# Optimization experiments

Hardware: AMD Instinct MI355X
Metric: run time of the kernel (lower is better)

## Reference

```python
import jax, jax.numpy as jnp
import numpy as np

BETA, ALPHA, NS_STEPS = 0.9, 1.0, 1
D_MODEL, D_STATE, D_CONV, EXPAND = 768, 16, 4, 2
D_INNER = EXPAND * D_MODEL
DT_RANK = -(-D_MODEL // 16)  # ceil(d_model/16) = 48
B, L = 2, 1024


def setup_inputs() -> dict:
    key = jax.random.key(0)
    ks = jax.random.split(key, 8)
    s = lambda k, shape, sc=0.02: jax.random.normal(k, shape, jnp.float32) * sc
    return {
        "hidden_states": jax.random.normal(ks[0], (B, L, D_MODEL), jnp.float32),
        "in_proj_w": s(ks[1], (2 * D_INNER, D_MODEL)),
        "conv_w": s(ks[2], (D_INNER, 1, D_CONV), 0.2),
        "conv_b": jnp.zeros((D_INNER,), jnp.float32),
        "x_proj_w": s(ks[3], (DT_RANK + 2 * D_STATE, D_INNER)),
        "dt_head_w": s(ks[4], (D_INNER, DT_RANK)),
        "dt_head_b": s(ks[5], (D_INNER,), 0.1),
        "out_proj_w": s(ks[6], (D_MODEL, D_INNER)),
        "D": jnp.ones((D_INNER,), jnp.float32),
    }


def _newton_schulz(G, steps):
    """Muon-style quintic Newton-Schulz orthogonalization of (b, d, n) with d >= n."""
    a, b, c = 3.4445, -4.7750, 2.0315
    X = G / (jnp.linalg.norm(G, axis=(-2, -1), keepdims=True) + 1e-7)
    X = X.swapaxes(-2, -1)  # (b, n, d): rows <= cols
    for _ in range(steps):
        A = X @ X.swapaxes(-2, -1)       # (b, n, n) small Gram
        Bm = b * A + c * (A @ A)
        X = a * X + Bm @ X
    return X.swapaxes(-2, -1)            # back to (b, d, n)


def reference(hidden_states, in_proj_w, conv_w, conv_b, x_proj_w, dt_head_w, dt_head_b, out_proj_w, D):
    Bz, Lz, _ = hidden_states.shape
    dtype = hidden_states.dtype
    # input projection -> x, z  (B, L, d_inner) each
    xz = jnp.einsum('bld,ed->ble', hidden_states, in_proj_w)
    x, z = jnp.split(xz, 2, axis=-1)
    # causal depthwise conv over time + SiLU
    xc = jax.lax.conv_general_dilated(
        x.swapaxes(1, 2), conv_w, (1,), [(D_CONV - 1, 0)],
        dimension_numbers=('NCH', 'OIH', 'NCH'), feature_group_count=D_INNER)
    x = jax.nn.silu(xc.swapaxes(1, 2) + conv_b)  # (B, L, d_inner)
    # projections for dt / k / q
    x_dbl = jnp.einsum('bld,ed->ble', x, x_proj_w)
    dt_low, k, q = jnp.split(x_dbl, [DT_RANK, DT_RANK + D_STATE], axis=-1)
    dt = jnp.einsum('blr,dr->bld', dt_low, dt_head_w)  # (B, L, d_inner), bias applied in scan

    def step(carry, inp):
        v, h = carry  # velocity / hidden states, each (b, d_inner, d_state)
        x_t, dt_t, k_t, q_t = inp
        dt_t = jax.nn.sigmoid(dt_t + dt_head_b)                              # (b, d)
        dt_t = dt_t / (1.0 + dt_t * jnp.sum(k_t * k_t, axis=-1, keepdims=True))
        dA = 1.0 - dt_t[:, :, None] * (k_t * k_t)[:, None, :]                # (b, d, n)
        G = (dt_t * x_t)[:, :, None] * k_t[:, None, :]                       # dt * u * k
        v = BETA * v + ALPHA * _newton_schulz(G, NS_STEPS)
        h = dA * h + v
        y_t = jnp.einsum('bdn,bn->bd', h, q_t) + D * x_t
        return (v, h), y_t

    init = (jnp.zeros((Bz, D_INNER, D_STATE), dtype),
            jnp.zeros((Bz, D_INNER, D_STATE), dtype))
    xs = (x.swapaxes(0, 1), dt.swapaxes(0, 1), k.swapaxes(0, 1), q.swapaxes(0, 1))
    _, y = jax.lax.scan(step, init, xs)        # (L, B, d_inner)
    y = y.swapaxes(0, 1) * jax.nn.silu(z)      # gate
    return jnp.einsum('bld,od->blo', y, out_proj_w)
```

## Files before the change

### kernel.cpp

```cpp
#include <hip/hip_runtime.h>

#define D_MODEL 768
#define D_STATE 16
#define D_INNER 1536
#define DT_RANK 48
#define NB 2
#define LSEQ 1024
#define NROWS (NB * LSEQ)
#define CCH 16
#define CLEN (LSEQ / CCH)
#define STP 16
#define BETA_CL 1.1790185e-03f
#define OUT_ELEMS (NROWS * D_MODEL)

typedef __attribute__((ext_vector_type(4))) float f32x4;
typedef __attribute__((ext_vector_type(8))) short s16x8;
typedef __attribute__((ext_vector_type(8))) unsigned short u16x8;
typedef __attribute__((ext_vector_type(4))) unsigned short u16x4;

__device__ __forceinline__ unsigned short f2bu(float f) {
  unsigned int x = __builtin_bit_cast(unsigned int, f);
  x += 0x7fffu + ((x >> 16) & 1u);
  return (unsigned short)(x >> 16);
}

typedef __attribute__((address_space(3))) unsigned int as3u32;
typedef __attribute__((address_space(1))) const unsigned int as1u32;
__device__ __forceinline__ void gload16(const unsigned short* g, unsigned short* l) {
  __builtin_amdgcn_global_load_lds((as1u32*)g, (as3u32*)l, 16, 0, 0);
}

#define CVT_TOTAL 663552
#define Z1_GROUPS 20480
__global__ __launch_bounds__(256) void cvt5z_kernel(const float* __restrict__ s0,
                                                    const float* __restrict__ s1,
                                                    const float* __restrict__ s2,
                                                    const float* __restrict__ s3,
                                                    const float* __restrict__ s4,
                                                    unsigned short* __restrict__ d0,
                                                    unsigned short* __restrict__ d1,
                                                    unsigned short* __restrict__ d2,
                                                    unsigned short* __restrict__ d3,
                                                    unsigned short* __restrict__ d4,
                                                    float* __restrict__ z1) {
  int g = blockIdx.x * 256 + threadIdx.x;
  if (g >= CVT_TOTAL) {
    int zg = g - CVT_TOTAL;
    f32x4 zero = {0.f, 0.f, 0.f, 0.f};
    if (zg < Z1_GROUPS) {
      *(f32x4*)(z1 + zg * 8) = zero;
      *(f32x4*)(z1 + zg * 8 + 4) = zero;
    }
    return;
  }
  const float* s;
  unsigned short* d;
  int base;
  if (g < 196608)      { s = s0; d = d0; base = 0; }
  else if (g < 491520) { s = s1; d = d1; base = 196608; }
  else if (g < 506880) { s = s2; d = d2; base = 491520; }
  else if (g < 516096) { s = s3; d = d3; base = 506880; }
  else                 { s = s4; d = d4; base = 516096; }
  int i = (g - base) * 8;
  f32x4 a = *(const f32x4*)(s + i);
  f32x4 b = *(const f32x4*)(s + i + 4);
  u16x8 o;
#pragma unroll
  for (int j = 0; j < 4; j++) { o[j] = f2bu(a[j]); o[4 + j] = f2bu(b[j]); }
  *(u16x8*)(d + i) = o;
}

template <bool PARTIAL>
__global__ __launch_bounds__(256) void gemm128(const unsigned short* __restrict__ A,
                                               const unsigned short* __restrict__ B,
                                               float* __restrict__ C, int K,
                                               int lda, int ldb, int ldc, int kseg_len) {
  __shared__ __align__(16) unsigned short As[2][128 * 32];
  __shared__ __align__(16) unsigned short Bs[2][128 * 32];
  const int m0 = blockIdx.y * 128, n0 = blockIdx.x * 128;
  const int kbeg = blockIdx.z * kseg_len;
  const int kend = kbeg + kseg_len;
  const int t = threadIdx.x;
  const int wave = t >> 6, lane = t & 63;
  const int wm = wave >> 1, wn = wave & 1;
  const int quad = lane >> 4, l16 = lane & 15;
  const int srow = lane >> 2;
  const int kcol = (lane & 3) * 8;

  float* Cp = C;
  if constexpr (PARTIAL) Cp = C + (size_t)blockIdx.z * (size_t)gridDim.y * 128 * ldc;

  auto stage = [&](int bi, int k0) {
#pragma unroll
    for (int r = 0; r < 2; r++) {
      const int seg = r * 64 + wave * 16;
      gload16(A + (size_t)(m0 + seg + srow) * lda + k0 + kcol, &As[bi][seg * 32]);
      gload16(B + (size_t)(n0 + seg + srow) * ldb + k0 + kcol, &Bs[bi][seg * 32]);
    }
  };

  f32x4 acc[4][4] = {};
  stage(0, kbeg);
  __syncthreads();
  int buf = 0;
  for (int k0 = kbeg; k0 < kend; k0 += 32) {
    if (k0 + 32 < kend) stage(buf ^ 1, k0 + 32);
    s16x8 af[4], bf[4];
#pragma unroll
    for (int i = 0; i < 4; i++) {
      af[i] = *(const s16x8*)&As[buf][(wm * 64 + i * 16 + l16) * 32 + quad * 8];
      bf[i] = *(const s16x8*)&Bs[buf][(wn * 64 + i * 16 + l16) * 32 + quad * 8];
    }
#pragma unroll
    for (int mi = 0; mi < 4; mi++)
#pragma unroll
      for (int ni = 0; ni < 4; ni++)
        acc[mi][ni] = __builtin_amdgcn_mfma_f32_16x16x32_bf16(af[mi], bf[ni], acc[mi][ni], 0, 0, 0);
    __syncthreads();
    buf ^= 1;
  }
#pragma unroll
  for (int mi = 0; mi < 4; mi++)
#pragma unroll
    for (int ni = 0; ni < 4; ni++)
#pragma unroll
      for (int r = 0; r < 4; r++) {
        int row = m0 + wm * 64 + mi * 16 + quad * 4 + r;
        int col = n0 + wn * 64 + ni * 16 + l16;
        Cp[(size_t)row * ldc + col] = acc[mi][ni][r];
      }
}

__global__ __launch_bounds__(256) void reduce4_kernel(const float* __restrict__ part,
                                                      float* __restrict__ out) {
  int i4 = (blockIdx.x * 256 + threadIdx.x) * 4;
  f32x4 a = *(const f32x4*)(part + i4);
  f32x4 b = *(const f32x4*)(part + (size_t)OUT_ELEMS + i4);
  f32x4 c = *(const f32x4*)(part + (size_t)2 * OUT_ELEMS + i4);
  f32x4 d = *(const f32x4*)(part + (size_t)3 * OUT_ELEMS + i4);
  f32x4 o;
#pragma unroll
  for (int j = 0; j < 4; j++) o[j] = (a[j] + b[j]) + (c[j] + d[j]);
  *(f32x4*)(out + i4) = o;
}

template <bool AF32, bool ATOMIC>
__global__ __launch_bounds__(256) void gemm_bt(const void* __restrict__ Av,
                                               const unsigned short* __restrict__ B,
                                               float* __restrict__ C, int M, int N, int K,
                                               int lda, int ldb, int ldc, int kseg_len) {
  __shared__ __align__(16) unsigned short As[2][64][40];
  __shared__ __align__(16) unsigned short Bs[2][64][40];
  const int m0 = blockIdx.y * 64, n0 = blockIdx.x * 64;
  const int kbeg = blockIdx.z * kseg_len;
  const int kend = (kbeg + kseg_len < K) ? (kbeg + kseg_len) : K;
  const int t = threadIdx.x;
  const int wave = t >> 6, lane = t & 63;
  const int wm = wave >> 1, wn = wave & 1;
  const int quad = lane >> 4, l16 = lane & 15;
  const int srow = t >> 2;
  const int kseg = (t & 3) * 8;
  const bool va = (m0 + srow) < M, vb = (n0 + srow) < N;
  const float* Af = (const float*)Av;
  const unsigned short* Ab = (const unsigned short*)Av;
  const unsigned short* Bp = B + (size_t)(n0 + srow) * ldb;

  f32x4 ra0, ra1;
  u16x8 rab, rbb;
  auto pref = [&](int k0) {
    const int kk = k0 + kseg;
    const int krem = kend - kk;
    if constexpr (AF32) {
      const float* Ap = Af + (size_t)(m0 + srow) * lda + kk;
      if (va && krem >= 8) {
        ra0 = *(const f32x4*)Ap;
        ra1 = *(const f32x4*)(Ap + 4);
      } else {
#pragma unroll
        for (int j = 0; j < 4; j++) {
          ra0[j] = (va && j < krem) ? Ap[j] : 0.0f;
          ra1[j] = (va && j + 4 < krem) ? Ap[j + 4] : 0.0f;
        }
      }
    } else {
      const unsigned short* Ap = Ab + (size_t)(m0 + srow) * lda + kk;
      if (va && krem >= 8) {
        rab = *(const u16x8*)Ap;
      } else {
#pragma unroll
        for (int j = 0; j < 8; j++) rab[j] = (va && j < krem) ? Ap[j] : (unsigned short)0;
      }
    }
    if (vb && krem >= 8) {
      rbb = *(const u16x8*)(Bp + kk);
    } else {
#pragma unroll
      for (int j = 0; j < 8; j++) rbb[j] = (vb && j < krem) ? Bp[kk + j] : (unsigned short)0;
    }
  };
  auto tolds = [&](int bi) {
    if constexpr (AF32) {
      u16x8 oa;
#pragma unroll
      for (int j = 0; j < 4; j++) { oa[j] = f2bu(ra0[j]); oa[4 + j] = f2bu(ra1[j]); }
      *(u16x8*)&As[bi][srow][kseg] = oa;
    } else {
      *(u16x8*)&As[bi][srow][kseg] = rab;
    }
    *(u16x8*)&Bs[bi][srow][kseg] = rbb;
  };

  f32x4 acc[2][2] = {};
  pref(kbeg);
  tolds(0);
  __syncthreads();
  int buf = 0;
  for (int k0 = kbeg; k0 < kend; k0 += 32) {
    const bool more = (k0 + 32 < kend);
    if (more) pref(k0 + 32);
    s16x8 a0 = *(const s16x8*)&As[buf][wm * 32 + l16][quad * 8];
    s16x8 a1 = *(const s16x8*)&As[buf][wm * 32 + 16 + l16][quad * 8];
    s16x8 b0 = *(const s16x8*)&Bs[buf][wn * 32 + l16][quad * 8];
    s16x8 b1 = *(const s16x8*)&Bs[buf][wn * 32 + 16 + l16][quad * 8];
    acc[0][0] = __builtin_amdgcn_mfma_f32_16x16x32_bf16(a0, b0, acc[0][0], 0, 0, 0);
    acc[0][1] = __builtin_amdgcn_mfma_f32_16x16x32_bf16(a0, b1, acc[0][1], 0, 0, 0);
    acc[1][0] = __builtin_amdgcn_mfma_f32_16x16x32_bf16(a1, b0, acc[1][0], 0, 0, 0);
    acc[1][1] = __builtin_amdgcn_mfma_f32_16x16x32_bf16(a1, b1, acc[1][1], 0, 0, 0);
    if (more) tolds(buf ^ 1);
    __syncthreads();
    buf ^= 1;
  }
#pragma unroll
  for (int mi = 0; mi < 2; mi++)
#pragma unroll
    for (int ni = 0; ni < 2; ni++)
#pragma unroll
      for (int r = 0; r < 4; r++) {
        int row = m0 + wm * 32 + mi * 16 + quad * 4 + r;
        int col = n0 + wn * 32 + ni * 16 + l16;
        if (row < M && col < N) {
          if constexpr (ATOMIC)
            atomicAdd(&C[(size_t)row * ldc + col], acc[mi][ni][r]);
          else
            C[(size_t)row * ldc + col] = acc[mi][ni][r];
        }
      }
}

__global__ __launch_bounds__(256) void conv_silu_kernel(const float* __restrict__ xzp,
                                                        const float* __restrict__ cw,
                                                        const float* __restrict__ cb,
                                                        float* __restrict__ xc,
                                                        unsigned short* __restrict__ xcb) {
  int g = blockIdx.x * 256 + threadIdx.x;
  int c4 = (g % 384) * 4;
  int row = g / 384;
  int l = row & (LSEQ - 1);
  const float* x0 = xzp;
  const float* x1 = xzp + (size_t)NROWS * 3072;
  f32x4 acc = *(const f32x4*)(cb + c4);
  f32x4 w[4];
#pragma unroll
  for (int ci = 0; ci < 4; ci++) w[ci] = *(const f32x4*)(cw + (c4 + ci) * 4);
#pragma unroll
  for (int j = 0; j < 4; j++) {
    int dl = l - 3 + j;
    if (dl >= 0) {
      size_t off = (size_t)(row - 3 + j) * 3072 + c4;
      f32x4 a0 = *(const f32x4*)(x0 + off);
      f32x4 a1 = *(const f32x4*)(x1 + off);
#pragma unroll
      for (int ci = 0; ci < 4; ci++) acc[ci] = fmaf(a0[ci] + a1[ci], w[ci][j], acc[ci]);
    }
  }
  f32x4 val;
  u16x4 ob;
#pragma unroll
  for (int ci = 0; ci < 4; ci++) {
    float sg = 1.0f / (1.0f + expf(-acc[ci]));
    val[ci] = acc[ci] * sg;
    ob[ci] = f2bu(val[ci]);
  }
  *(f32x4*)(xc + (size_t)row * D_INNER + c4) = val;
  *(u16x4*)(xcb + (size_t)row * D_INNER + c4) = ob;
}

__global__ __launch_bounds__(256) void precompute_kernel(const float* __restrict__ xdbl,
                                                         float* __restrict__ dtbuf,
                                                         const float* __restrict__ xconv,
                                                         const float* __restrict__ dtb,
                                                         float* __restrict__ gammabuf,
                                                         float* __restrict__ kqbuf) {
  int row = blockIdx.x;
  int t = threadIdx.x;
  const float* xr = xdbl + (size_t)row * 80;
  float nk = 0.0f;
#pragma unroll
  for (int n = 0; n < 16; n++) { float kv = xr[48 + n]; nk += kv * kv; }
  float nupart = 0.0f;
#pragma unroll
  for (int gi = 0; gi < 2; gi++) {
    int g = gi * 256 + t;
    if (g < 384) {
      int d = g * 4;
      f32x4 draw = *(const f32x4*)(dtbuf + (size_t)row * D_INNER + d);
      f32x4 bb = *(const f32x4*)(dtb + d);
      f32x4 xcv = *(const f32x4*)(xconv + (size_t)row * D_INNER + d);
      f32x4 df;
#pragma unroll
      for (int j = 0; j < 4; j++) {
        float sg = 1.0f / (1.0f + expf(-(draw[j] + bb[j])));
        float dv = sg / (1.0f + sg * nk);
        df[j] = dv;
        float u = dv * xcv[j];
        nupart += u * u;
      }
      *(f32x4*)(dtbuf + (size_t)row * D_INNER + d) = df;
    }
  }
  __shared__ float red[4];
  float v = nupart;
#pragma unroll
  for (int off = 32; off > 0; off >>= 1) v += __shfl_xor(v, off);
  if ((t & 63) == 0) red[t >> 6] = v;
  __syncthreads();
  float nu = red[0] + red[1] + red[2] + red[3];
  float p = nu * nk;
  float s = sqrtf(p) + 1e-7f;
  float tt = p / (s * s);
  float gamma = (3.4445f + tt * (-4.7750f + 2.0315f * tt)) / s;
  if (t == 0) gammabuf[row] = gamma;
  if (t < 8)
    *(f32x4*)(kqbuf + (size_t)row * 32 + t * 4) = *(const f32x4*)(xr + 48 + t * 4);
}

__global__ __launch_bounds__(256) void scan_phase1(const float* __restrict__ xconv,
                                                   const float* __restrict__ dtbuf,
                                                   const float* __restrict__ kqbuf,
                                                   const float* __restrict__ gammabuf,
                                                   float* __restrict__ cvp,
                                                   float* __restrict__ chp,
                                                   float* __restrict__ gp,
                                                   float* __restrict__ rp) {
  __shared__ __align__(16) float xc_s[2][STP][64];
  __shared__ __align__(16) float dt_s[2][STP][64];
  __shared__ __align__(16) float kq_s[2][STP][36];
  __shared__ float g_s[2][STP];
  const int t = threadIdx.x;
  const int nq = t & 3, dloc = t >> 2;
  const int b = blockIdx.x / (24 * CCH);
  const int rem = blockIdx.x % (24 * CCH);
  const int d0 = (rem / CCH) * 64;
  const int c = rem % CCH;
  const int tbase = c * CLEN;
  const size_t ub = ((size_t)b * LSEQ + tbase) * D_INNER + d0;
  const float* kqb = kqbuf + ((size_t)b * LSEQ + tbase) * 32;
  const float* gmb = gammabuf + (size_t)b * LSEQ + tbase;
  const int prow = t >> 4, pcol = (t & 15) * 4;
  const int krow = t >> 3, kcol = (t & 7) * 4;
  f32x4 pxc, pd, pk;
  float pg;
  auto prefetch = [&](int t0) {
    size_t off = ub + (size_t)(t0 + prow) * D_INNER + pcol;
    pxc = *(const f32x4*)(xconv + off);
    pd = *(const f32x4*)(dtbuf + off);
    if (t < 128) pk = *(const f32x4*)(kqb + (size_t)(t0 + krow) * 32 + kcol);
    if (t < STP) pg = gmb[t0 + t];
  };
  auto writelds = [&](int bi) {
    *(f32x4*)&xc_s[bi][prow][pcol] = pxc;
    *(f32x4*)&dt_s[bi][prow][pcol] = pd;
    if (t < 128) *(f32x4*)&kq_s[bi][krow][kcol] = pk;
    if (t < STP) g_s[bi][t] = pg;
  };
  f32x4 v = {0.f, 0.f, 0.f, 0.f}, h = {0.f, 0.f, 0.f, 0.f};
  f32x4 g = {0.f, 0.f, 0.f, 0.f}, r = {1.f, 1.f, 1.f, 1.f};
  float bt = 0.9f;
  prefetch(0);
  writelds(0);
  __syncthreads();
  int buf = 0;
  for (int t0 = 0; t0 < CLEN; t0 += STP) {
    const bool more = (t0 + STP < CLEN);
    if (more) prefetch(t0 + STP);
#pragma unroll 4
    for (int s = 0; s < STP; s++) {
      float dtf = dt_s[buf][s][dloc];
      float u = g_s[buf][s] * dtf * xc_s[buf][s][dloc];
#pragma unroll
      for (int j = 0; j < 4; j++) {
        float kj = kq_s[buf][s][nq * 4 + j];
        v[j] = fmaf(0.9f, v[j], u * kj);
        float a = fmaf(-dtf * kj, kj, 1.0f);
        h[j] = fmaf(a, h[j], v[j]);
        r[j] *= a;
        g[j] = fmaf(a, g[j], bt);
      }
      bt *= 0.9f;
    }
    if (more) writelds(buf ^ 1);
    __syncthreads();
    buf ^= 1;
  }
  size_t o = (((size_t)b * CCH + c) * D_INNER + d0 + dloc) * 16 + nq * 4;
  *(f32x4*)(cvp + o) = v;
  *(f32x4*)(chp + o) = h;
  *(f32x4*)(gp + o) = g;
  *(f32x4*)(rp + o) = r;
}

__global__ __launch_bounds__(256) void scan_phase2(const float* __restrict__ cvp,
                                                   const float* __restrict__ chp,
                                                   float* __restrict__ gp,
                                                   float* __restrict__ rp) {
  int i4 = (blockIdx.x * 256 + threadIdx.x) * 4;
  int b = i4 / (D_INNER * 16);
  int rem = i4 % (D_INNER * 16);
  f32x4 v0 = {0.f, 0.f, 0.f, 0.f}, h0 = {0.f, 0.f, 0.f, 0.f};
#pragma unroll
  for (int c = 0; c < CCH; c++) {
    size_t o = ((size_t)(b * CCH + c)) * (D_INNER * 16) + rem;
    f32x4 cv = *(const f32x4*)(cvp + o);
    f32x4 ch = *(const f32x4*)(chp + o);
    f32x4 gg = *(const f32x4*)(gp + o);
    f32x4 rr = *(const f32x4*)(rp + o);
    *(f32x4*)(gp + o) = v0;
    *(f32x4*)(rp + o) = h0;
#pragma unroll
    for (int j = 0; j < 4; j++) {
      float v0n = fmaf(BETA_CL, v0[j], cv[j]);
      float h0n = fmaf(gg[j], v0[j], fmaf(rr[j], h0[j], ch[j]));
      v0[j] = v0n;
      h0[j] = h0n;
    }
  }
}

__global__ __launch_bounds__(256) void scan_phase3(const float* __restrict__ dtbuf,
                                                   const float* __restrict__ kqbuf,
                                                   const float* __restrict__ gammabuf,
                                                   const float* __restrict__ gp,
                                                   const float* __restrict__ rp,
                                                   const float* __restrict__ xconv,
                                                   const float* __restrict__ xzp,
                                                   const float* __restrict__ Dp,
                                                   unsigned short* __restrict__ ygb) {
  __shared__ __align__(16) float xc_s[2][STP][64];
  __shared__ __align__(16) float dt_s[2][STP][64];
  __shared__ __align__(16) float z_s[2][STP][64];
  __shared__ __align__(16) float kq_s[2][STP][36];
  __shared__ float g_s[2][STP];
  const int t = threadIdx.x;
  const int nq = t & 3, dloc = t >> 2;
  const int b = blockIdx.x / (24 * CCH);
  const int rem = blockIdx.x % (24 * CCH);
  const int d0 = (rem / CCH) * 64;
  const int c = rem % CCH;
  const int tbase = c * CLEN;
  const size_t ub = ((size_t)b * LSEQ + tbase) * D_INNER + d0;
  const float* kqb = kqbuf + ((size_t)b * LSEQ + tbase) * 32;
  const float* gmb = gammabuf + (size_t)b * LSEQ + tbase;
  const float* z0 = xzp + ((size_t)b * LSEQ + tbase) * 3072 + 1536 + d0;
  const float* z1 = z0 + (size_t)NROWS * 3072;
  unsigned short* y_p = ygb + (size_t)b * LSEQ * D_INNER + d0 + dloc;
  const int prow = t >> 4, pcol = (t & 15) * 4;
  const int krow = t >> 3, kcol = (t & 7) * 4;
  f32x4 pxc, pd, pz, pk;
  float pg;
  auto prefetch = [&](int t0) {
    size_t off = ub + (size_t)(t0 + prow) * D_INNER + pcol;
    pxc = *(const f32x4*)(xconv + off);
    pd = *(const f32x4*)(dtbuf + off);
    size_t zoff = (size_t)(t0 + prow) * 3072 + pcol;
    f32x4 a0 = *(const f32x4*)(z0 + zoff);
    f32x4 a1 = *(const f32x4*)(z1 + zoff);
#pragma unroll
    for (int j = 0; j < 4; j++) pz[j] = a0[j] + a1[j];
    if (t < 128) pk = *(const f32x4*)(kqb + (size_t)(t0 + krow) * 32 + kcol);
    if (t < STP) pg = gmb[t0 + t];
  };
  auto writelds = [&](int bi) {
    *(f32x4*)&xc_s[bi][prow][pcol] = pxc;
    *(f32x4*)&dt_s[bi][prow][pcol] = pd;
    *(f32x4*)&z_s[bi][prow][pcol] = pz;
    if (t < 128) *(f32x4*)&kq_s[bi][krow][kcol] = pk;
    if (t < STP) g_s[bi][t] = pg;
  };
  size_t so = (((size_t)b * CCH + c) * D_INNER + d0 + dloc) * 16 + nq * 4;
  f32x4 v = *(const f32x4*)(gp + so);
  f32x4 h = *(const f32x4*)(rp + so);
  const float Dd = Dp[d0 + dloc];
  prefetch(0);
  writelds(0);
  __syncthreads();
  int buf = 0;
  for (int t0 = 0; t0 < CLEN; t0 += STP) {
    const bool more = (t0 + STP < CLEN);
    if (more) prefetch(t0 + STP);
#pragma unroll 4
    for (int s = 0; s < STP; s++) {
      float xcv = xc_s[buf][s][dloc];
      float dtf = dt_s[buf][s][dloc];
      float u = g_s[buf][s] * dtf * xcv;
      f32x4 kv = *(const f32x4*)&kq_s[buf][s][nq * 4];
      f32x4 qv = *(const f32x4*)&kq_s[buf][s][16 + nq * 4];
      float yp = 0.0f;
#pragma unroll
      for (int j = 0; j < 4; j++) {
        float kj = kv[j];
        v[j] = fmaf(0.9f, v[j], u * kj);
        float dA = fmaf(-dtf * kj, kj, 1.0f);
        h[j] = fmaf(dA, h[j], v[j]);
        yp = fmaf(h[j], qv[j], yp);
      }
      yp += __shfl_xor(yp, 1);
      yp += __shfl_xor(yp, 2);
      float zv = z_s[buf][s][dloc];
      float sz = zv / (1.0f + expf(-zv));
      float val = (yp + Dd * xcv) * sz;
      if (nq == 0) y_p[(size_t)(tbase + t0 + s) * D_INNER] = f2bu(val);
    }
    if (more) writelds(buf ^ 1);
    __syncthreads();
    buf ^= 1;
  }
}

extern "C" void kernel_launch(void* const* d_in, const int* in_sizes, int n_in,
                              void* d_out, int out_size, void* d_ws, size_t ws_size,
                              hipStream_t stream) {
  const float* hidden = (const float*)d_in[0];
  const float* w_in   = (const float*)d_in[1];
  const float* conv_w = (const float*)d_in[2];
  const float* conv_b = (const float*)d_in[3];
  const float* w_x    = (const float*)d_in[4];
  const float* w_dt   = (const float*)d_in[5];
  const float* b_dt   = (const float*)d_in[6];
  const float* w_out  = (const float*)d_in[7];
  const float* Dp     = (const float*)d_in[8];

  float* ws    = (float*)d_ws;
  float* xzp   = ws;
  float* xconv = xzp + (size_t)2 * NROWS * 3072;
  float* xdbl  = xconv + (size_t)NROWS * D_INNER;
  float* dtbuf = xdbl + (size_t)NROWS * 80;
  float* gammabuf = dtbuf + (size_t)NROWS * D_INNER;
  float* kqbuf = gammabuf + NROWS;
  const size_t PL = (size_t)NB * CCH * D_INNER * 16;
  float* cvp   = kqbuf + (size_t)NROWS * 32;
  float* chp   = cvp + PL;
  float* gp    = chp + PL;
  float* rp    = gp + PL;
  float* opart = rp + PL;
  unsigned short* bfr = (unsigned short*)(opart + (size_t)4 * OUT_ELEMS);
  unsigned short* hbf = bfr;
  unsigned short* wib = hbf + 1572864;
  unsigned short* wxb = wib + 2359296;
  unsigned short* wdb = wxb + 122880;
  unsigned short* wob = wdb + 73728;
  unsigned short* xcb = wob + 1179648;
  unsigned short* ygb = xcb + 3145728;

  dim3 blk(256);
  cvt5z_kernel<<<dim3((CVT_TOTAL + Z1_GROUPS) / 256), blk, 0, stream>>>(
      hidden, w_in, w_x, w_dt, w_out, hbf, wib, wxb, wdb, wob, xdbl);
  gemm128<true><<<dim3(24, 16, 2), blk, 0, stream>>>(hbf, wib, xzp, 768, 768, 768, 3072, 384);
  conv_silu_kernel<<<dim3(3072), blk, 0, stream>>>(xzp, conv_w, conv_b, xconv, xcb);
  gemm_bt<false, true><<<dim3(2, 32, 8), blk, 0, stream>>>(xcb, wxb, xdbl, 2048, 80, 1536,
                                                           1536, 1536, 80, 192);
  gemm_bt<true, false><<<dim3(24, 32, 1), blk, 0, stream>>>(xdbl, wdb, dtbuf, 2048, 1536, 48,
                                                            80, 48, 1536, 48);
  precompute_kernel<<<dim3(NROWS), blk, 0, stream>>>(xdbl, dtbuf, xconv, b_dt, gammabuf, kqbuf);
  scan_phase1<<<dim3(NB * 24 * CCH), blk, 0, stream>>>(xconv, dtbuf, kqbuf, gammabuf,
                                                       cvp, chp, gp, rp);
  scan_phase2<<<dim3(48), blk, 0, stream>>>(cvp, chp, gp, rp);
  scan_phase3<<<dim3(NB * 24 * CCH), blk, 0, stream>>>(dtbuf, kqbuf, gammabuf, gp, rp,
                                                       xconv, xzp, Dp, ygb);
  gemm128<true><<<dim3(6, 16, 4), blk, 0, stream>>>(ygb, wob, opart, 1536,
                                                    1536, 1536, 768, 384);
  reduce4_kernel<<<dim3(OUT_ELEMS / 1024), blk, 0, stream>>>(opart, (float*)d_out);
}
```

Measured before the change: 212.8 us.

## Drop split-K on input projection and fuse dt sigmoid into dt GEMM epilogue

The input-projection GEMM now runs without split-K, writing a single xz buffer instead of two partial buffers that conv and scan_phase3 had to load and add. The sigmoid/normalisation of dt is moved into the epilogue of the dt GEMM, with per-row k-norms computed into shared memory, so the precompute kernel no longer reads and rewrites dtbuf. This removes a large partial buffer's traffic and one full read-modify-write pass over dt. In exchange the input GEMM launches half as many blocks, which may lower occupancy.

```diff
diff --git a/kernel.cpp b/kernel.cpp
--- a/kernel.cpp
+++ b/kernel.cpp
@@ -144,13 +144,15 @@
   *(f32x4*)(out + i4) = o;
 }
 
-template <bool AF32, bool ATOMIC>
+template <bool AF32, bool ATOMIC, bool DTF>
 __global__ __launch_bounds__(256) void gemm_bt(const void* __restrict__ Av,
                                                const unsigned short* __restrict__ B,
                                                float* __restrict__ C, int M, int N, int K,
-                                               int lda, int ldb, int ldc, int kseg_len) {
+                                               int lda, int ldb, int ldc, int kseg_len,
+                                               const float* __restrict__ dtb) {
   __shared__ __align__(16) unsigned short As[2][64][40];
   __shared__ __align__(16) unsigned short Bs[2][64][40];
+  __shared__ float nk_s[64];
   const int m0 = blockIdx.y * 64, n0 = blockIdx.x * 64;
   const int kbeg = blockIdx.z * kseg_len;
   const int kend = (kbeg + kseg_len < K) ? (kbeg + kseg_len) : K;
@@ -213,6 +215,15 @@
   f32x4 acc[2][2] = {};
   pref(kbeg);
   tolds(0);
+  if constexpr (DTF) {
+    if (t < 64 && (m0 + t) < M) {
+      const float* kr = Af + (size_t)(m0 + t) * lda + 48;
+      float nk = 0.0f;
+#pragma unroll
+      for (int n = 0; n < 16; n++) nk += kr[n] * kr[n];
+      nk_s[t] = nk;
+    }
+  }
   __syncthreads();
   int buf = 0;
   for (int k0 = kbeg; k0 < kend; k0 += 32) {
@@ -239,15 +250,20 @@
         int row = m0 + wm * 32 + mi * 16 + quad * 4 + r;
         int col = n0 + wn * 32 + ni * 16 + l16;
         if (row < M && col < N) {
+          float cv = acc[mi][ni][r];
+          if constexpr (DTF) {
+            float sg = 1.0f / (1.0f + expf(-(cv + dtb[col])));
+            cv = sg / (1.0f + sg * nk_s[row - m0]);
+          }
           if constexpr (ATOMIC)
-            atomicAdd(&C[(size_t)row * ldc + col], acc[mi][ni][r]);
+            atomicAdd(&C[(size_t)row * ldc + col], cv);
           else
-            C[(size_t)row * ldc + col] = acc[mi][ni][r];
+            C[(size_t)row * ldc + col] = cv;
         }
       }
 }
 
-__global__ __launch_bounds__(256) void conv_silu_kernel(const float* __restrict__ xzp,
+__global__ __launch_bounds__(256) void conv_silu_kernel(const float* __restrict__ xz,
                                                         const float* __restrict__ cw,
                                                         const float* __restrict__ cb,
                                                         float* __restrict__ xc,
@@ -256,8 +272,6 @@
   int c4 = (g % 384) * 4;
   int row = g / 384;
   int l = row & (LSEQ - 1);
-  const float* x0 = xzp;
-  const float* x1 = xzp + (size_t)NROWS * 3072;
   f32x4 acc = *(const f32x4*)(cb + c4);
   f32x4 w[4];
 #pragma unroll
@@ -266,11 +280,9 @@
   for (int j = 0; j < 4; j++) {
     int dl = l - 3 + j;
     if (dl >= 0) {
-      size_t off = (size_t)(row - 3 + j) * 3072 + c4;
-      f32x4 a0 = *(const f32x4*)(x0 + off);
-      f32x4 a1 = *(const f32x4*)(x1 + off);
-#pragma unroll
-      for (int ci = 0; ci < 4; ci++) acc[ci] = fmaf(a0[ci] + a1[ci], w[ci][j], acc[ci]);
+      f32x4 xv = *(const f32x4*)(xz + (size_t)(row - 3 + j) * 3072 + c4);
+#pragma unroll
+      for (int ci = 0; ci < 4; ci++) acc[ci] = fmaf(xv[ci], w[ci][j], acc[ci]);
     }
   }
   f32x4 val;
@@ -285,12 +297,11 @@
   *(u16x4*)(xcb + (size_t)row * D_INNER + c4) = ob;
 }
 
-__global__ __launch_bounds__(256) void precompute_kernel(const float* __restrict__ xdbl,
-                                                         float* __restrict__ dtbuf,
-                                                         const float* __restrict__ xconv,
-                                                         const float* __restrict__ dtb,
-                                                         float* __restrict__ gammabuf,
-                                                         float* __restrict__ kqbuf) {
+__global__ __launch_bounds__(256) void gamma_kernel(const float* __restrict__ xdbl,
+                                                    const float* __restrict__ dtfbuf,
+                                                    const float* __restrict__ xconv,
+                                                    float* __restrict__ gammabuf,
+                                                    float* __restrict__ kqbuf) {
   int row = blockIdx.x;
   int t = threadIdx.x;
   const float* xr = xdbl + (size_t)row * 80;
@@ -303,19 +314,13 @@
     int g = gi * 256 + t;
     if (g < 384) {
       int d = g * 4;
-      f32x4 draw = *(const f32x4*)(dtbuf + (size_t)row * D_INNER + d);
-      f32x4 bb = *(const f32x4*)(dtb + d);
+      f32x4 df = *(const f32x4*)(dtfbuf + (size_t)row * D_INNER + d);
       f32x4 xcv = *(const f32x4*)(xconv + (size_t)row * D_INNER + d);
-      f32x4 df;
 #pragma unroll
       for (int j = 0; j < 4; j++) {
-        float sg = 1.0f / (1.0f + expf(-(draw[j] + bb[j])));
-        float dv = sg / (1.0f + sg * nk);
-        df[j] = dv;
-        float u = dv * xcv[j];
+        float u = df[j] * xcv[j];
         nupart += u * u;
       }
-      *(f32x4*)(dtbuf + (size_t)row * D_INNER + d) = df;
     }
   }
   __shared__ float red[4];
@@ -442,7 +447,7 @@
                                                    const float* __restrict__ gp,
                                                    const float* __restrict__ rp,
                                                    const float* __restrict__ xconv,
-                                                   const float* __restrict__ xzp,
+                                                   const float* __restrict__ xz,
                                                    const float* __restrict__ Dp,
                                                    unsigned short* __restrict__ ygb) {
   __shared__ __align__(16) float xc_s[2][STP][64];
@@ -460,8 +465,7 @@
   const size_t ub = ((size_t)b * LSEQ + tbase) * D_INNER + d0;
   const float* kqb = kqbuf + ((size_t)b * LSEQ + tbase) * 32;
   const float* gmb = gammabuf + (size_t)b * LSEQ + tbase;
-  const float* z0 = xzp + ((size_t)b * LSEQ + tbase) * 3072 + 1536 + d0;
-  const float* z1 = z0 + (size_t)NROWS * 3072;
+  const float* z0 = xz + ((size_t)b * LSEQ + tbase) * 3072 + 1536 + d0;
   unsigned short* y_p = ygb + (size_t)b * LSEQ * D_INNER + d0 + dloc;
   const int prow = t >> 4, pcol = (t & 15) * 4;
   const int krow = t >> 3, kcol = (t & 7) * 4;
@@ -471,11 +475,7 @@
     size_t off = ub + (size_t)(t0 + prow) * D_INNER + pcol;
     pxc = *(const f32x4*)(xconv + off);
     pd = *(const f32x4*)(dtbuf + off);
-    size_t zoff = (size_t)(t0 + prow) * 3072 + pcol;
-    f32x4 a0 = *(const f32x4*)(z0 + zoff);
-    f32x4 a1 = *(const f32x4*)(z1 + zoff);
-#pragma unroll
-    for (int j = 0; j < 4; j++) pz[j] = a0[j] + a1[j];
+    pz = *(const f32x4*)(z0 + (size_t)(t0 + prow) * 3072 + pcol);
     if (t < 128) pk = *(const f32x4*)(kqb + (size_t)(t0 + krow) * 32 + kcol);
     if (t < STP) pg = gmb[t0 + t];
   };
@@ -540,8 +540,8 @@
   const float* Dp     = (const float*)d_in[8];
 
   float* ws    = (float*)d_ws;
-  float* xzp   = ws;
-  float* xconv = xzp + (size_t)2 * NROWS * 3072;
+  float* xz    = ws;
+  float* xconv = xz + (size_t)NROWS * 3072;
   float* xdbl  = xconv + (size_t)NROWS * D_INNER;
   float* dtbuf = xdbl + (size_t)NROWS * 80;
   float* gammabuf = dtbuf + (size_t)NROWS * D_INNER;
@@ -564,18 +564,18 @@
   dim3 blk(256);
   cvt5z_kernel<<<dim3((CVT_TOTAL + Z1_GROUPS) / 256), blk, 0, stream>>>(
       hidden, w_in, w_x, w_dt, w_out, hbf, wib, wxb, wdb, wob, xdbl);
-  gemm128<true><<<dim3(24, 16, 2), blk, 0, stream>>>(hbf, wib, xzp, 768, 768, 768, 3072, 384);
-  conv_silu_kernel<<<dim3(3072), blk, 0, stream>>>(xzp, conv_w, conv_b, xconv, xcb);
-  gemm_bt<false, true><<<dim3(2, 32, 8), blk, 0, stream>>>(xcb, wxb, xdbl, 2048, 80, 1536,
-                                                           1536, 1536, 80, 192);
-  gemm_bt<true, false><<<dim3(24, 32, 1), blk, 0, stream>>>(xdbl, wdb, dtbuf, 2048, 1536, 48,
-                                                            80, 48, 1536, 48);
-  precompute_kernel<<<dim3(NROWS), blk, 0, stream>>>(xdbl, dtbuf, xconv, b_dt, gammabuf, kqbuf);
+  gemm128<false><<<dim3(24, 16, 1), blk, 0, stream>>>(hbf, wib, xz, 768, 768, 768, 3072, 768);
+  conv_silu_kernel<<<dim3(3072), blk, 0, stream>>>(xz, conv_w, conv_b, xconv, xcb);
+  gemm_bt<false, true, false><<<dim3(2, 32, 8), blk, 0, stream>>>(
+      xcb, wxb, xdbl, 2048, 80, 1536, 1536, 1536, 80, 192, nullptr);
+  gemm_bt<true, false, true><<<dim3(24, 32, 1), blk, 0, stream>>>(
+      xdbl, wdb, dtbuf, 2048, 1536, 48, 80, 48, 1536, 48, b_dt);
+  gamma_kernel<<<dim3(NROWS), blk, 0, stream>>>(xdbl, dtbuf, xconv, gammabuf, kqbuf);
   scan_phase1<<<dim3(NB * 24 * CCH), blk, 0, stream>>>(xconv, dtbuf, kqbuf, gammabuf,
                                                        cvp, chp, gp, rp);
   scan_phase2<<<dim3(48), blk, 0, stream>>>(cvp, chp, gp, rp);
   scan_phase3<<<dim3(NB * 24 * CCH), blk, 0, stream>>>(dtbuf, kqbuf, gammabuf, gp, rp,
-                                                       xconv, xzp, Dp, ygb);
+                                                       xconv, xz, Dp, ygb);
   gemm128<true><<<dim3(6, 16, 4), blk, 0, stream>>>(ygb, wob, opart, 1536,
                                                     1536, 1536, 768, 384);
   reduce4_kernel<<<dim3(OUT_ELEMS / 1024), blk, 0, stream>>>(opart, (float*)d_out);
```

New measurement: 204.3 us. 1.04x faster.
